# Performance work log

Hardware: AMD Instinct MI355X
Metric: run time of the kernel (lower is better)

## Reference

```python
import jax, jax.numpy as jnp
import numpy as np

B, T, L, D, H = 4, 512, 15, 2048, 1024
PRUNE_RATIO = 0.4
K = int(np.ceil(T * PRUNE_RATIO))  # max spans kept per doc = 205


def setup_inputs() -> dict:
    key = jax.random.key(0)
    ks = jax.random.split(key, 8)
    span_vecs = jax.random.normal(ks[0], (B, T, L, D), jnp.float32)
    # binary validity mask over candidate spans
    span_mask = (jax.random.uniform(ks[1], (B, T, L)) > 0.15).astype(jnp.float32)
    begin = jnp.broadcast_to(jnp.arange(T, dtype=jnp.int32)[None, :, None], (B, T, L))
    end = begin + jnp.arange(L, dtype=jnp.int32)[None, None, :]
    sequence_lengths = jax.random.randint(ks[2], (B,), T // 2, T + 1).astype(jnp.int32)
    s = 0.02
    W1 = jax.random.normal(ks[3], (D, H), jnp.float32) * s
    W2 = jax.random.normal(ks[4], (H, H), jnp.float32) * s
    W3 = jax.random.normal(ks[5], (H, 1), jnp.float32) * s
    return {
        'span_vecs': span_vecs, 'span_mask': span_mask,
        'span_begin': begin, 'span_end': end,
        'sequence_lengths': sequence_lengths,
        'W1': W1, 'b1': jnp.zeros((H,), jnp.float32),
        'W2': W2, 'b2': jnp.zeros((H,), jnp.float32),
        'W3': W3, 'b3': jnp.zeros((1,), jnp.float32),
    }


def reference(span_vecs, span_mask, span_begin, span_end, sequence_lengths,
              W1, b1, W2, b2, W3, b3):
    # MLP scorer (dropout is identity in eval mode)
    h = jax.nn.relu(jnp.einsum('btld,dh->btlh', span_vecs, W1) + b1)
    h = jax.nn.relu(jnp.einsum('btlh,hg->btlg', h, W2) + b2)
    scores = jnp.einsum('btlh,ho->btlo', h, W3) + b3            # [B,T,L,1]
    prune_scores = scores - (1.0 - span_mask[..., None]) * 10000.0

    # prune_spans: per-doc top-k over all T*L candidates, k = ceil(ratio*seq_len)
    flat = prune_scores.reshape(B, T * L)
    span_lengths = jnp.ceil(sequence_lengths.astype(jnp.float32) * PRUNE_RATIO).astype(jnp.int32)
    _, top_idx = jax.lax.top_k(flat, K)                          # [B,K]
    top_idx = jnp.sort(top_idx, axis=1)                          # sort_after_pruning=True

    # filter_spans: gather along flattened span axis
    def gather(x):
        xf = x.reshape(B, T * L, -1)
        return jnp.take_along_axis(xf, top_idx[:, :, None], axis=1)

    f_vecs = gather(span_vecs)                                   # [B,K,D]
    f_scores = gather(prune_scores)                              # [B,K,1]
    f_begin = gather(span_begin[..., None])                      # [B,K,1] int
    f_end = gather(span_end[..., None])                          # [B,K,1] int

    # create_masks: square validity mask and lower-triangular mask
    valid = (jnp.arange(K)[None, :] < span_lengths[:, None]).astype(jnp.float32)  # [B,K]
    square_mask = valid[:, :, None] * valid[:, None, :]          # [B,K,K]
    triangular_mask = square_mask * jnp.tril(jnp.ones((K, K), jnp.float32))[None]

    return (prune_scores, top_idx, f_vecs, f_scores, f_begin, f_end,
            span_lengths, square_mask, triangular_mask)
```

## Files before the change

kernel.cpp:

```cpp
#include <hip/hip_runtime.h>
#include <stdint.h>

#define B_ 4
#define T_ 512
#define L_ 15
#define D_ 2048
#define H_ 1024
#define TL_ (T_*L_)
#define M_ (B_*TL_)
#define K_SPANS 205
#define NSORT 8192
#define NPART 16

#define OFF_PRUNE 0
#define OFF_TOP   (OFF_PRUNE + M_)
#define OFF_FVECS (OFF_TOP + B_*K_SPANS)
#define OFF_FSC   (OFF_FVECS + B_*K_SPANS*D_)
#define OFF_FBEG  (OFF_FSC + B_*K_SPANS)
#define OFF_FEND  (OFF_FBEG + B_*K_SPANS)
#define OFF_SL    (OFF_FEND + B_*K_SPANS)
#define OFF_SQ    (OFF_SL + B_)
#define OFF_TRI   (OFF_SQ + B_*K_SPANS*K_SPANS)

typedef __attribute__((ext_vector_type(8))) short s16x8;
typedef __attribute__((ext_vector_type(4))) float f32x4;

__device__ __forceinline__ ushort bf16rne(float f) {
    uint u = __float_as_uint(f);
    return (ushort)((u + 0x7fffu + ((u >> 16) & 1u)) >> 16);
}
__device__ __forceinline__ float bfval(ushort h) {
    return __uint_as_float(((uint)h) << 16);
}
__device__ __forceinline__ void split1(float x, ushort& h0, ushort& h1, ushort& h2) {
    h0 = bf16rne(x);            float f0 = bfval(h0);
    float r = x - f0;           h1 = bf16rne(r);
    float r2 = r - bfval(h1);   h2 = bf16rne(r2);
}
__device__ __forceinline__ void split4(float4 v, uint2& q0, uint2& q1, uint2& q2) {
    ushort a0[4], a1[4], a2[4];
    float x[4] = {v.x, v.y, v.z, v.w};
    #pragma unroll
    for (int j = 0; j < 4; ++j) split1(x[j], a0[j], a1[j], a2[j]);
    q0 = make_uint2((uint)a0[0] | ((uint)a0[1] << 16), (uint)a0[2] | ((uint)a0[3] << 16));
    q1 = make_uint2((uint)a1[0] | ((uint)a1[1] << 16), (uint)a1[2] | ((uint)a1[3] << 16));
    q2 = make_uint2((uint)a2[0] | ((uint)a2[1] << 16), (uint)a2[2] | ((uint)a2[3] << 16));
}
__device__ __forceinline__ void split2(float x, ushort& h0, ushort& h1) {
    h0 = bf16rne(x);            float f0 = bfval(h0);
    h1 = bf16rne(x - f0);
}
__device__ __forceinline__ void split4_2(float4 v, uint2& q0, uint2& q1) {
    ushort a0[4], a1[4];
    float x[4] = {v.x, v.y, v.z, v.w};
    #pragma unroll
    for (int j = 0; j < 4; ++j) split2(x[j], a0[j], a1[j]);
    q0 = make_uint2((uint)a0[0] | ((uint)a0[1] << 16), (uint)a0[2] | ((uint)a0[3] << 16));
    q1 = make_uint2((uint)a1[0] | ((uint)a1[1] << 16), (uint)a1[2] | ((uint)a1[3] << 16));
}

__device__ __forceinline__ f32x4 mfma16(s16x8 a, s16x8 b, f32x4 c) {
    return __builtin_amdgcn_mfma_f32_16x16x32_bf16(a, b, c, 0, 0, 0);
}


template<int K32>
__global__ __launch_bounds__(256) void split_a_panel(
    const float* __restrict__ A, ushort* __restrict__ P0,
    ushort* __restrict__ P1)
{
    const int l    = threadIdx.x & 63;
    const int w    = threadIdx.x >> 6;
    const int tile = blockIdx.x * 4 + w;
    const int r16  = tile / K32;
    const int g    = tile % K32;
    const int row  = r16 * 16 + (l & 15);
    const int k0   = g * 32 + (l >> 4) * 8;
    const float* src = A + (size_t)row * (K32 * 32) + k0;
    float4 v0 = *(const float4*)src;
    float4 v1 = *(const float4*)(src + 4);
    uint2 a0, a1, b0, b1;
    split4_2(v0, a0, a1);
    split4_2(v1, b0, b1);
    const size_t off = ((size_t)tile * 64 + l) * 8;
    *(uint4*)(P0 + off) = make_uint4(a0.x, a0.y, b0.x, b0.y);
    *(uint4*)(P1 + off) = make_uint4(a1.x, a1.y, b1.x, b1.y);
}

template<int K32>
__global__ __launch_bounds__(256) void split_w_frag(
    const float* __restrict__ W, ushort* __restrict__ P0,
    ushort* __restrict__ P1)
{
    const int idx  = blockIdx.x * 256 + threadIdx.x;
    const int l    = idx & 63;
    const int tile = idx >> 6;
    const int n16  = tile / K32;
    const int g    = tile % K32;
    const int n    = n16 * 16 + (l & 15);
    const int kb   = g * 32 + (l >> 4) * 8;
    ushort h0[8], h1[8];
    #pragma unroll
    for (int j = 0; j < 8; ++j) {
        float wv = W[(size_t)(kb + j) * 1024 + n];
        split2(wv, h0[j], h1[j]);
    }
    const size_t off = (size_t)idx * 8;
    *(uint4*)(P0 + off) = *(uint4*)h0;
    *(uint4*)(P1 + off) = *(uint4*)h1;
}

template<int K32, bool FUSE>
__global__ __launch_bounds__(256, 2) void gemm_frag(
    const ushort* __restrict__ Ap0, const ushort* __restrict__ Ap1,
    const ushort* __restrict__ Bp0, const ushort* __restrict__ Bp1,
    const float* __restrict__ bias, const float* __restrict__ W3,
    float* __restrict__ out)
{
    const int tid = threadIdx.x;
    const int l   = tid & 63;
    const int w   = tid >> 6;
    const int lr  = l & 15;
    const int lq  = l >> 4;
    const int mb  = blockIdx.y * 16 + w * 4;
    const int nb  = blockIdx.x * 4;
    const int n0  = blockIdx.x * 64;

    size_t aoff[4], boff[4];
    #pragma unroll
    for (int t = 0; t < 4; ++t) {
        aoff[t] = ((size_t)(mb + t) * K32 * 64 + l) * 8;
        boff[t] = ((size_t)(nb + t) * K32 * 64 + l) * 8;
    }

    f32x4 acc[4][4] = {};

    const int rot = ((w + blockIdx.x + blockIdx.y) & 3) * (K32 / 4);

    for (int gi = 0; gi < K32; ++gi) {
        int g = gi + rot;
        g -= (g >= K32) ? K32 : 0;
        s16x8 A0[4], A1[4], B0[4], B1[4];
        const size_t gofs = (size_t)g * 512;
        #pragma unroll
        for (int t = 0; t < 4; ++t) {
            const size_t ao = aoff[t] + gofs;
            const size_t bo = boff[t] + gofs;
            A0[t] = *(const s16x8*)(Ap0 + ao);
            A1[t] = *(const s16x8*)(Ap1 + ao);
            B0[t] = *(const s16x8*)(Bp0 + bo);
            B1[t] = *(const s16x8*)(Bp1 + bo);
        }
        #pragma unroll
        for (int mt = 0; mt < 4; ++mt)
            #pragma unroll
            for (int nt = 0; nt < 4; ++nt) {
                f32x4 c = acc[mt][nt];
                c = mfma16(A0[mt], B0[nt], c);
                c = mfma16(A0[mt], B1[nt], c);
                c = mfma16(A1[mt], B0[nt], c);
                c = mfma16(A1[mt], B1[nt], c);
                acc[mt][nt] = c;
            }
    }

    float bv[4];
    #pragma unroll
    for (int nt = 0; nt < 4; ++nt) bv[nt] = bias[n0 + nt * 16 + lr];

    if (!FUSE) {
        #pragma unroll
        for (int mt = 0; mt < 4; ++mt)
            #pragma unroll
            for (int nt = 0; nt < 4; ++nt)
                #pragma unroll
                for (int r = 0; r < 4; ++r) {
                    const int row = (mb + mt) * 16 + lq * 4 + r;
                    out[(size_t)row * 1024 + n0 + nt * 16 + lr] =
                        fmaxf(acc[mt][nt][r] + bv[nt], 0.f);
                }
    } else {
        float wv[4];
        #pragma unroll
        for (int nt = 0; nt < 4; ++nt) wv[nt] = W3[n0 + nt * 16 + lr];
        #pragma unroll
        for (int mt = 0; mt < 4; ++mt)
            #pragma unroll
            for (int r = 0; r < 4; ++r) {
                float v = 0.f;
                #pragma unroll
                for (int nt = 0; nt < 4; ++nt)
                    v += fmaxf(acc[mt][nt][r] + bv[nt], 0.f) * wv[nt];
                v += __shfl_xor(v, 1);
                v += __shfl_xor(v, 2);
                v += __shfl_xor(v, 4);
                v += __shfl_xor(v, 8);
                if (lr == 0)
                    out[(size_t)blockIdx.x * M_ + (mb + mt) * 16 + lq * 4 + r] = v;
            }
    }
}

__global__ void split_w_panel(const float* __restrict__ W, ushort* __restrict__ P0,
                              ushort* __restrict__ P1, ushort* __restrict__ P2, int K8)
{
    const int idx = blockIdx.x * 256 + threadIdx.x;
    if (idx >= K8 * 1024) return;
    const int k8 = idx >> 10;
    const int n  = idx & 1023;
    ushort h0[8], h1[8], h2[8];
    #pragma unroll
    for (int j = 0; j < 8; ++j) {
        float w = W[(size_t)(k8 * 8 + j) * 1024 + n];
        split1(w, h0[j], h1[j], h2[j]);
    }
    *(uint4*)(P0 + (size_t)idx * 8) = *(uint4*)h0;
    *(uint4*)(P1 + (size_t)idx * 8) = *(uint4*)h1;
    *(uint4*)(P2 + (size_t)idx * 8) = *(uint4*)h2;
}

template<int KDIM, bool FUSE>
__global__ __launch_bounds__(256, 2) void gemm_split(
    const float* __restrict__ A,
    const ushort* __restrict__ P0, const ushort* __restrict__ P1,
    const ushort* __restrict__ P2,
    const float* __restrict__ bias, const float* __restrict__ W3,
    float* __restrict__ out)
{
    __shared__ ushort aLds[3][4 * 257 * 8];
    __shared__ ushort bLds[3][4 * 65 * 8];

    const int tid   = threadIdx.x;
    const int lane  = tid & 63;
    const int lr    = lane & 15;
    const int lq    = lane >> 4;
    const int waveM = (tid >> 6) * 64;
    const int m0    = blockIdx.y * 256;
    const int n0    = blockIdx.x * 64;

    const int bq = tid >> 6;
    const int bn = tid & 63;
    const int ar = tid >> 3;
    const int ac4 = tid & 7;

    f32x4 acc[4][4] = {};

    for (int kt = 0; kt < KDIM / 32; ++kt) {
        const int k80 = kt * 4;
        const size_t bchunk = ((size_t)(k80 + bq) * 1024 + n0 + bn) * 8;
        uint4 bf0 = *(const uint4*)(P0 + bchunk);
        uint4 bf1 = *(const uint4*)(P1 + bchunk);
        uint4 bf2 = *(const uint4*)(P2 + bchunk);
        float4 av[8];
        #pragma unroll
        for (int sw = 0; sw < 8; ++sw) {
            const int row = sw * 32 + ar;
            av[sw] = *(const float4*)(A + (size_t)(m0 + row) * KDIM + kt * 32 + ac4 * 4);
        }
        __syncthreads();
        *(uint4*)&bLds[0][(bq * 65 + bn) * 8] = bf0;
        *(uint4*)&bLds[1][(bq * 65 + bn) * 8] = bf1;
        *(uint4*)&bLds[2][(bq * 65 + bn) * 8] = bf2;
        #pragma unroll
        for (int sw = 0; sw < 8; ++sw) {
            const int row = sw * 32 + ar;
            uint2 q0, q1, q2;
            split4(av[sw], q0, q1, q2);
            const int off = ((ac4 >> 1) * 257 + row) * 8 + (ac4 & 1) * 4;
            *(uint2*)&aLds[0][off] = q0;
            *(uint2*)&aLds[1][off] = q1;
            *(uint2*)&aLds[2][off] = q2;
        }
        __syncthreads();

        s16x8 B0[4], B1[4], B2[4];
        #pragma unroll
        for (int nt = 0; nt < 4; ++nt) {
            const int boff = (lq * 65 + nt * 16 + lr) * 8;
            B0[nt] = *(const s16x8*)&bLds[0][boff];
            B1[nt] = *(const s16x8*)&bLds[1][boff];
            B2[nt] = *(const s16x8*)&bLds[2][boff];
        }
        #pragma unroll
        for (int mt = 0; mt < 4; ++mt) {
            const int aoff = (lq * 257 + waveM + mt * 16 + lr) * 8;
            s16x8 A0 = *(const s16x8*)&aLds[0][aoff];
            s16x8 A1 = *(const s16x8*)&aLds[1][aoff];
            s16x8 A2 = *(const s16x8*)&aLds[2][aoff];
            #pragma unroll
            for (int nt = 0; nt < 4; ++nt) {
                f32x4 c = acc[mt][nt];
                c = mfma16(A0, B0[nt], c);
                c = mfma16(A0, B1[nt], c);
                c = mfma16(A1, B0[nt], c);
                c = mfma16(A1, B1[nt], c);
                c = mfma16(A0, B2[nt], c);
                c = mfma16(A2, B0[nt], c);
                acc[mt][nt] = c;
            }
        }
    }

    float bv[4];
    #pragma unroll
    for (int nt = 0; nt < 4; ++nt) bv[nt] = bias[n0 + nt * 16 + lr];

    if (!FUSE) {
        #pragma unroll
        for (int mt = 0; mt < 4; ++mt)
            #pragma unroll
            for (int nt = 0; nt < 4; ++nt)
                #pragma unroll
                for (int r = 0; r < 4; ++r) {
                    const int row = m0 + waveM + mt * 16 + lq * 4 + r;
                    out[(size_t)row * 1024 + n0 + nt * 16 + lr] =
                        fmaxf(acc[mt][nt][r] + bv[nt], 0.f);
                }
    } else {
        float wv[4];
        #pragma unroll
        for (int nt = 0; nt < 4; ++nt) wv[nt] = W3[n0 + nt * 16 + lr];
        #pragma unroll
        for (int mt = 0; mt < 4; ++mt)
            #pragma unroll
            for (int r = 0; r < 4; ++r) {
                float v = 0.f;
                #pragma unroll
                for (int nt = 0; nt < 4; ++nt)
                    v += fmaxf(acc[mt][nt][r] + bv[nt], 0.f) * wv[nt];
                v += __shfl_xor(v, 1);
                v += __shfl_xor(v, 2);
                v += __shfl_xor(v, 4);
                v += __shfl_xor(v, 8);
                if (lr == 0)
                    out[(size_t)blockIdx.x * M_ + m0 + waveM + mt * 16 + lq * 4 + r] = v;
            }
    }
}

__device__ __forceinline__ uint64_t score_key(float s, int idx) {
    unsigned u = __float_as_uint(s);
    u = (u & 0x80000000u) ? ~u : (u | 0x80000000u);
    return ((uint64_t)u << 32) | (uint64_t)(0xFFFFFFFFu - (unsigned)idx);
}

__device__ __forceinline__ float compute_score(
    const float* __restrict__ partial, const float* __restrict__ mask,
    float b3v, int b, int i)
{
    const int m = b * TL_ + i;
    float s = b3v;
    #pragma unroll
    for (int cb = 0; cb < NPART; ++cb) s += partial[(size_t)cb * M_ + m];
    s -= (1.0f - mask[m]) * 10000.0f;
    return s;
}

__global__ __launch_bounds__(1024) void topk_kernel(
    const float* __restrict__ partial, const float* __restrict__ span_mask,
    const int* __restrict__ span_begin, const int* __restrict__ span_end,
    const int* __restrict__ seq_len, const float* __restrict__ b3,
    float* __restrict__ out, int* __restrict__ topk_ws)
{
    __shared__ uint64_t keys[NSORT];
    const int tid = threadIdx.x;
    const int b   = blockIdx.x;
    const float b3v = b3[0];

    for (int i = tid; i < NSORT; i += 1024) {
        if (i < TL_) {
            float s = compute_score(partial, span_mask, b3v, b, i);
            out[OFF_PRUNE + b * TL_ + i] = s;
            keys[i] = score_key(s, i);
        } else {
            keys[i] = 0ull;
        }
    }
    __syncthreads();

    for (unsigned kk = 2; kk <= NSORT; kk <<= 1) {
        for (unsigned j = kk >> 1; j > 0; j >>= 1) {
            for (unsigned i = (unsigned)tid; i < NSORT; i += 1024) {
                unsigned ixj = i ^ j;
                if (ixj > i) {
                    uint64_t x = keys[i], y = keys[ixj];
                    bool desc = ((i & kk) == 0);
                    if (desc ? (x < y) : (x > y)) { keys[i] = y; keys[ixj] = x; }
                }
            }
            __syncthreads();
        }
    }

    const uint64_t cutoff = keys[K_SPANS - 1];
    __syncthreads();

    unsigned* sScan = (unsigned*)keys;
    unsigned base = 0;
    const unsigned lane = tid & 63;
    const unsigned wv   = tid >> 6;
    for (int c = 0; c < TL_; c += 1024) {
        const int i = c + tid;
        bool flag = false; float s = 0.f;
        if (i < TL_) {
            s = compute_score(partial, span_mask, b3v, b, i);
            flag = (score_key(s, i) >= cutoff);
        }
        uint64_t bal = __ballot(flag);
        unsigned pre = (unsigned)__popcll(bal & ((1ull << lane) - 1ull));
        if (lane == 0) sScan[wv] = (unsigned)__popcll(bal);
        __syncthreads();
        unsigned woff = 0, tot = 0;
        for (int w = 0; w < 16; ++w) {
            unsigned v = sScan[w];
            if (w < (int)wv) woff += v;
            tot += v;
        }
        if (flag) {
            const int g = b * K_SPANS + (int)(base + woff + pre);
            topk_ws[g]        = i;
            out[OFF_TOP + g]  = (float)i;
            out[OFF_FSC + g]  = s;
            out[OFF_FBEG + g] = (float)span_begin[b * TL_ + i];
            out[OFF_FEND + g] = (float)span_end[b * TL_ + i];
        }
        base += tot;
        __syncthreads();
    }

    if (tid == 0)
        out[OFF_SL + b] = ceilf(0.4f * (float)seq_len[b]);
}

__global__ void gather_vecs(const float* __restrict__ span_vecs,
                            const int* __restrict__ topk_ws,
                            float* __restrict__ out)
{
    const int bk  = blockIdx.x;
    const int b   = bk / K_SPANS;
    const int row = topk_ws[bk];
    const float4* src = (const float4*)(span_vecs + ((size_t)b * TL_ + row) * D_);
    float4* dst = (float4*)(out + OFF_FVECS + (size_t)bk * D_);
    for (int j = threadIdx.x; j < D_ / 4; j += blockDim.x) dst[j] = src[j];
}

__global__ void masks_kernel(const int* __restrict__ seq_len,
                             float* __restrict__ out)
{
    const int idx = blockIdx.x * blockDim.x + threadIdx.x;
    if (idx >= B_ * K_SPANS * K_SPANS) return;
    const int b = idx / (K_SPANS * K_SPANS);
    const int r = idx - b * K_SPANS * K_SPANS;
    const int i = r / K_SPANS;
    const int j = r - i * K_SPANS;
    const int sl = (int)ceilf(0.4f * (float)seq_len[b]);
    const float v = (i < sl && j < sl) ? 1.0f : 0.0f;
    out[OFF_SQ + idx]  = v;
    out[OFF_TRI + idx] = (j <= i) ? v : 0.0f;
}

extern "C" void kernel_launch(void* const* d_in, const int* in_sizes, int n_in,
                              void* d_out, int out_size, void* d_ws, size_t ws_size,
                              hipStream_t stream)
{
    const float* span_vecs  = (const float*)d_in[0];
    const float* span_mask  = (const float*)d_in[1];
    const int*   span_begin = (const int*)  d_in[2];
    const int*   span_end   = (const int*)  d_in[3];
    const int*   seq_len    = (const int*)  d_in[4];
    const float* W1 = (const float*)d_in[5];
    const float* b1 = (const float*)d_in[6];
    const float* W2 = (const float*)d_in[7];
    const float* b2 = (const float*)d_in[8];
    const float* W3 = (const float*)d_in[9];
    const float* b3 = (const float*)d_in[10];
    float* out = (float*)d_out;

    const size_t A1CH = (size_t)M_ * D_;
    const size_t H1CH = (size_t)M_ * H_;
    const size_t W1CH = (size_t)D_ * H_;
    const size_t W2CH = (size_t)H_ * H_;
    const size_t FAST_NEED =
        2 * A1CH * 2 + (size_t)M_ * H_ * 4 + 2 * H1CH * 2 +
        2 * W1CH * 2 + 2 * W2CH * 2 + (size_t)NPART * M_ * 4 + 4096;

    float* partial;
    int*   topk_ws;

    if (ws_size >= FAST_NEED) {
        char* p = (char*)d_ws;
        ushort* a1p0 = (ushort*)p;  p += A1CH * 2;
        ushort* a1p1 = (ushort*)p;  p += A1CH * 2;
        float*  h1   = (float*)p;   p += (size_t)M_ * H_ * 4;
        ushort* h1p0 = (ushort*)p;  p += H1CH * 2;
        ushort* h1p1 = (ushort*)p;  p += H1CH * 2;
        ushort* w1p0 = (ushort*)p;  p += W1CH * 2;
        ushort* w1p1 = (ushort*)p;  p += W1CH * 2;
        ushort* w2p0 = (ushort*)p;  p += W2CH * 2;
        ushort* w2p1 = (ushort*)p;  p += W2CH * 2;
        partial      = (float*)p;   p += (size_t)NPART * M_ * 4;
        topk_ws      = (int*)p;

        split_a_panel<64><<<(M_ / 16) * 64 / 4, 256, 0, stream>>>(
            span_vecs, a1p0, a1p1);
        split_w_frag<64><<<(H_ / 16) * 64 * 64 / 256, 256, 0, stream>>>(
            W1, w1p0, w1p1);
        split_w_frag<32><<<(H_ / 16) * 32 * 64 / 256, 256, 0, stream>>>(
            W2, w2p0, w2p1);

        gemm_frag<64, false><<<dim3(16, M_ / 256), 256, 0, stream>>>(
            a1p0, a1p1, w1p0, w1p1, b1, nullptr, h1);
        split_a_panel<32><<<(M_ / 16) * 32 / 4, 256, 0, stream>>>(
            h1, h1p0, h1p1);
        gemm_frag<32, true><<<dim3(16, M_ / 256), 256, 0, stream>>>(
            h1p0, h1p1, w2p0, w2p1, b2, W3, partial);
    } else {
        float*  h1   = (float*)d_ws;
        partial      = h1 + (size_t)M_ * H_;
        ushort* w1p0 = (ushort*)(partial + (size_t)NPART * M_);
        ushort* w1p1 = w1p0 + (size_t)256 * 1024 * 8;
        ushort* w1p2 = w1p1 + (size_t)256 * 1024 * 8;
        ushort* w2p0 = w1p2 + (size_t)256 * 1024 * 8;
        ushort* w2p1 = w2p0 + (size_t)128 * 1024 * 8;
        ushort* w2p2 = w2p1 + (size_t)128 * 1024 * 8;
        topk_ws      = (int*)(w2p2 + (size_t)128 * 1024 * 8);

        split_w_panel<<<(256 * 1024) / 256, 256, 0, stream>>>(W1, w1p0, w1p1, w1p2, 256);
        split_w_panel<<<(128 * 1024) / 256, 256, 0, stream>>>(W2, w2p0, w2p1, w2p2, 128);
        gemm_split<2048, false><<<dim3(16, 120), 256, 0, stream>>>(
            span_vecs, w1p0, w1p1, w1p2, b1, nullptr, h1);
        gemm_split<1024, true><<<dim3(16, 120), 256, 0, stream>>>(
            h1, w2p0, w2p1, w2p2, b2, W3, partial);
    }

    topk_kernel<<<B_, 1024, 0, stream>>>(
        partial, span_mask, span_begin, span_end, seq_len, b3, out, topk_ws);
    gather_vecs<<<B_ * K_SPANS, 256, 0, stream>>>(span_vecs, topk_ws, out);
    masks_kernel<<<(B_ * K_SPANS * K_SPANS + 255) / 256, 256, 0, stream>>>(
        seq_len, out);
}
```

Before: 1.208 ms.

## Fuse bf16 split-packing of hidden layer into first GEMM epilogue

The first GEMM's epilogue now stages its ReLU output tile in shared memory and writes it straight into the two-part bf16 fragment layout that the second GEMM consumes. This removes the fp32 h1 intermediate buffer and the separate split_a_panel pass, saving a full write and read of a large activation tensor. The top-k compaction pass also reads the already-stored prune scores instead of recomputing them from the partial sums. In exchange the epilogue gains shared-memory staging and block-wide barriers, and the fallback path's gemm_split calls were left unchanged even though gemm_frag's signature changed.

```diff
diff --git a/kernel.cpp b/kernel.cpp
--- a/kernel.cpp
+++ b/kernel.cpp
@@ -115,7 +115,8 @@
     const ushort* __restrict__ Ap0, const ushort* __restrict__ Ap1,
     const ushort* __restrict__ Bp0, const ushort* __restrict__ Bp1,
     const float* __restrict__ bias, const float* __restrict__ W3,
-    float* __restrict__ out)
+    float* __restrict__ outF, ushort* __restrict__ outP0,
+    ushort* __restrict__ outP1)
 {
     const int tid = threadIdx.x;
     const int l   = tid & 63;
@@ -169,16 +170,33 @@
     for (int nt = 0; nt < 4; ++nt) bv[nt] = bias[n0 + nt * 16 + lr];
 
     if (!FUSE) {
-        #pragma unroll
-        for (int mt = 0; mt < 4; ++mt)
+        __shared__ float sT[4][16][65];
+        const int KH32 = 32;
+        #pragma unroll
+        for (int mt = 0; mt < 4; ++mt) {
             #pragma unroll
             for (int nt = 0; nt < 4; ++nt)
                 #pragma unroll
-                for (int r = 0; r < 4; ++r) {
-                    const int row = (mb + mt) * 16 + lq * 4 + r;
-                    out[(size_t)row * 1024 + n0 + nt * 16 + lr] =
+                for (int r = 0; r < 4; ++r)
+                    sT[w][lq * 4 + r][nt * 16 + lr] =
                         fmaxf(acc[mt][nt][r] + bv[nt], 0.f);
+            __syncthreads();
+            const int r16 = mb + mt;
+            #pragma unroll
+            for (int gg = 0; gg < 2; ++gg) {
+                ushort h0[8], h1v[8];
+                #pragma unroll
+                for (int jj = 0; jj < 8; ++jj) {
+                    float v = sT[w][lr][gg * 32 + lq * 8 + jj];
+                    split2(v, h0[jj], h1v[jj]);
                 }
+                const size_t off =
+                    ((size_t)(r16 * KH32 + blockIdx.x * 2 + gg) * 64 + l) * 8;
+                *(uint4*)(outP0 + off) = *(uint4*)h0;
+                *(uint4*)(outP1 + off) = *(uint4*)h1v;
+            }
+            __syncthreads();
+        }
     } else {
         float wv[4];
         #pragma unroll
@@ -196,7 +214,7 @@
                 v += __shfl_xor(v, 4);
                 v += __shfl_xor(v, 8);
                 if (lr == 0)
-                    out[(size_t)blockIdx.x * M_ + (mb + mt) * 16 + lq * 4 + r] = v;
+                    outF[(size_t)blockIdx.x * M_ + (mb + mt) * 16 + lq * 4 + r] = v;
             }
     }
 }
@@ -403,7 +421,7 @@
         const int i = c + tid;
         bool flag = false; float s = 0.f;
         if (i < TL_) {
-            s = compute_score(partial, span_mask, b3v, b, i);
+            s = out[OFF_PRUNE + b * TL_ + i];
             flag = (score_key(s, i) >= cutoff);
         }
         uint64_t bal = __ballot(flag);
@@ -481,7 +499,7 @@
     const size_t W1CH = (size_t)D_ * H_;
     const size_t W2CH = (size_t)H_ * H_;
     const size_t FAST_NEED =
-        2 * A1CH * 2 + (size_t)M_ * H_ * 4 + 2 * H1CH * 2 +
+        2 * A1CH * 2 + 2 * H1CH * 2 +
         2 * W1CH * 2 + 2 * W2CH * 2 + (size_t)NPART * M_ * 4 + 4096;
 
     float* partial;
@@ -491,7 +509,6 @@
         char* p = (char*)d_ws;
         ushort* a1p0 = (ushort*)p;  p += A1CH * 2;
         ushort* a1p1 = (ushort*)p;  p += A1CH * 2;
-        float*  h1   = (float*)p;   p += (size_t)M_ * H_ * 4;
         ushort* h1p0 = (ushort*)p;  p += H1CH * 2;
         ushort* h1p1 = (ushort*)p;  p += H1CH * 2;
         ushort* w1p0 = (ushort*)p;  p += W1CH * 2;
@@ -509,11 +526,9 @@
             W2, w2p0, w2p1);
 
         gemm_frag<64, false><<<dim3(16, M_ / 256), 256, 0, stream>>>(
-            a1p0, a1p1, w1p0, w1p1, b1, nullptr, h1);
-        split_a_panel<32><<<(M_ / 16) * 32 / 4, 256, 0, stream>>>(
-            h1, h1p0, h1p1);
+            a1p0, a1p1, w1p0, w1p1, b1, nullptr, nullptr, h1p0, h1p1);
         gemm_frag<32, true><<<dim3(16, M_ / 256), 256, 0, stream>>>(
-            h1p0, h1p1, w2p0, w2p1, b2, W3, partial);
+            h1p0, h1p1, w2p0, w2p1, b2, W3, partial, nullptr, nullptr);
     } else {
         float*  h1   = (float*)d_ws;
         partial      = h1 + (size_t)M_ * H_;
```

After: 1.177 ms. 1.03x faster.
